# Optimization experiments

Hardware: AMD Instinct MI355X
Metric: run time of the kernel (lower is better)

## Reference

```python
import jax, jax.numpy as jnp
import numpy as np


def _gru_cell(x, h, Wih, Whh, bih, bhh):
    # torch nn.GRU cell math: gates ordered [r, z, n]
    gi = Wih @ x + bih
    gh = Whh @ h + bhh
    ir, iz, inn = jnp.split(gi, 3)
    hr, hz, hn = jnp.split(gh, 3)
    r = jax.nn.sigmoid(ir + hr)
    z = jax.nn.sigmoid(iz + hz)
    n = jnp.tanh(inn + r * hn)
    return (1.0 - z) * n + z * h


def _lrelu(x):
    # torch nn.LeakyReLU default negative_slope=0.01
    return jnp.where(x >= 0, x, 0.01 * x)


def setup_inputs() -> dict:
    key = jax.random.key(0)
    ks = jax.random.split(key, 24)
    V, E, H, C, S, T = 32000, 512, 1024, 2048, 256, 129
    w = lambda k, shape: jax.random.normal(k, shape, jnp.float32) * 0.02
    return {
        "inputs": jax.random.randint(ks[0], (T,), 0, V),
        "h1": jax.random.normal(ks[1], (H,), jnp.float32),
        "h2": jax.random.normal(ks[2], (H,), jnp.float32),
        "projected_keys": jax.random.normal(ks[3], (S, H), jnp.float32),
        "encoder_outputs": jax.random.normal(ks[4], (S, C), jnp.float32),
        "embeds": jax.random.normal(ks[5], (V, E), jnp.float32),
        "Wq": w(ks[6], (H, H)),
        "v_att": w(ks[7], (H,)),
        "W_ih1": w(ks[8], (3 * H, E + C)),
        "W_hh1": w(ks[9], (3 * H, H)),
        "b_ih1": w(ks[10], (3 * H,)),
        "b_hh1": w(ks[11], (3 * H,)),
        "W_ih2": w(ks[12], (3 * H, H + C)),
        "W_hh2": w(ks[13], (3 * H, H)),
        "b_ih2": w(ks[14], (3 * H,)),
        "b_hh2": w(ks[15], (3 * H,)),
        "W_pre": w(ks[16], (H, E + H + C)),
        "b_pre": w(ks[17], (H,)),
        "W_out": w(ks[18], (E, H)),
        "b_out": w(ks[19], (E,)),
    }


def reference(inputs, h1, h2, projected_keys, encoder_outputs, embeds, Wq, v_att,
              W_ih1, W_hh1, b_ih1, b_hh1, W_ih2, W_hh2, b_ih2, b_hh2,
              W_pre, b_pre, W_out, b_out):
    # teacher_forcing = 1.0 -> decoder input at step i is inputs[i] (ground truth)
    emb_seq = embeds[inputs[:-1]]  # [T-1, E]

    def step(carry, emb):
        h1, h2 = carry
        # additive attention: query from top-layer hidden state
        q = Wq @ h2                                     # [H]
        e = jnp.tanh(projected_keys + q) @ v_att        # [S]
        alphas = jax.nn.softmax(e)                      # [S]
        context = alphas @ encoder_outputs              # [C]
        h1n = _gru_cell(jnp.concatenate([emb, context]), h1, W_ih1, W_hh1, b_ih1, b_hh1)
        o1 = _lrelu(h1n)                                # dropout identity (eval)
        h2n = _gru_cell(jnp.concatenate([o1, context]), h2, W_ih2, W_hh2, b_ih2, b_hh2)
        o2 = _lrelu(h2n)
        pre = _lrelu(W_pre @ jnp.concatenate([emb, o2, context]) + b_pre)  # [H]
        out = W_out @ o2 + b_out                        # [E]
        return (h1n, h2n), (out, pre, alphas)

    (h1f, h2f), (outs, pres, alphas) = jax.lax.scan(step, (h1, h2), emb_seq)
    # torch.cat(outputs, dim=1) of [1,1,E] pieces -> [1, T-1, E]
    return outs[None], pres[None], alphas, h1f, h2f
```

## Files before the change

kernel.cpp:

```cpp
#include <hip/hip_runtime.h>

typedef unsigned int uint32;

#define GBLK 256
#define BT 512
#define NSTEP 128

#define CQ   0
#define CGH  1
#define CE   2
#define CCTX 3
#define CH1  4
#define CH2  5
#define QF    1024
#define EF    2048
#define CTXF  2304
#define H1FO  4352
#define H2FO  5376
#define O1F   6400
#define O2F   7424
#define GH1F  8448
#define GH2F  12544

struct Params {
  const int* inputs;
  const float *h1_in, *h2_in, *embeds, *vatt;
  const float *pk, *enc, *Wq, *Wih1, *Whh1, *Wih2, *Whh2, *Wpre, *Wout;
  const float *bih1, *bhh1, *bih2, *bhh2, *bpre, *bout;
  float* out;
  float* ws;
};

__device__ __forceinline__ float blo(uint32 u) { return __uint_as_float(u << 16); }
__device__ __forceinline__ float bhi(uint32 u) { return __uint_as_float(u & 0xffff0000u); }
__device__ __forceinline__ uint32 bfr(float f) {
  uint32 u = __float_as_uint(f);
  return (u + 0x7fffu + ((u >> 16) & 1u)) >> 16;
}

__device__ __forceinline__ float ald(const float* a) {
  return __hip_atomic_load(a, __ATOMIC_RELAXED, __HIP_MEMORY_SCOPE_AGENT);
}
__device__ __forceinline__ void ast(float* a, float v) {
  __hip_atomic_store(a, v, __ATOMIC_RELAXED, __HIP_MEMORY_SCOPE_AGENT);
}

__device__ __forceinline__ float4 cld16(const float* p) {
  float4 r;
  asm volatile("global_load_dwordx4 %0, %1, off sc0 sc1\n\ts_waitcnt vmcnt(0)"
               : "=&v"(r) : "v"(p) : "memory");
  return r;
}

#define VDRAIN() asm volatile("s_waitcnt vmcnt(0)" ::: "memory")

__device__ __forceinline__ void cadd(int* wsi, int c, int b) {
  __hip_atomic_fetch_add(wsi + c * 128 + (b & 7) * 16, 1,
                         __ATOMIC_RELAXED, __HIP_MEMORY_SCOPE_AGENT);
}
__device__ __forceinline__ void cpoll(const int* wsi, int c, int tgt) {
  const int* base = wsi + c * 128;
  for (;;) {
    bool ok = true;
#pragma unroll
    for (int k = 0; k < 8; ++k)
      ok &= (__hip_atomic_load(base + k * 16, __ATOMIC_RELAXED,
                               __HIP_MEMORY_SCOPE_AGENT) >= tgt);
    if (ok) return;
    __builtin_amdgcn_s_sleep(1);
  }
}

__device__ __forceinline__ float wsum(float v) {
#pragma unroll
  for (int o = 32; o; o >>= 1) v += __shfl_xor(v, o, 64);
  return v;
}

__device__ __forceinline__ void ldchunk(const float* W, size_t base, int lane, uint32* r) {
  const float* wf = W + base + lane * 8;
  float4 a = *(const float4*)wf;
  float4 c = *(const float4*)(wf + 4);
  r[0] = bfr(a.x) | (bfr(a.y) << 16);
  r[1] = bfr(a.z) | (bfr(a.w) << 16);
  r[2] = bfr(c.x) | (bfr(c.y) << 16);
  r[3] = bfr(c.z) | (bfr(c.w) << 16);
}

__device__ __forceinline__ float dotchunk(const uint32* r, const float* xc, int lane) {
  const float* x = xc + lane * 8;
  float4 x0 = *(const float4*)x, x1 = *(const float4*)(x + 4);
  return blo(r[0]) * x0.x + bhi(r[0]) * x0.y + blo(r[1]) * x0.z + bhi(r[1]) * x0.w +
         blo(r[2]) * x1.x + bhi(r[2]) * x1.y + blo(r[3]) * x1.z + bhi(r[3]) * x1.w;
}

__device__ __forceinline__ float sigm(float x) { return 1.f / (1.f + expf(-x)); }
__device__ __forceinline__ float lrelu(float x) { return x >= 0.f ? x : 0.01f * x; }

__global__ __launch_bounds__(BT, 2) void dec_cnt_kernel(Params p) {
  __shared__ float sx[8192];
  __shared__ float s_red[8];
  __shared__ float s_part[72];

  const int tid = threadIdx.x;
  const int lane = tid & 63;
  const int w = tid >> 6;
  const int b = blockIdx.x;
  const int gw = b * 8 + w;
  const int i0 = b * 4;
  const int j0 = b * 8;

  int* wsi = (int*)p.ws;

  float* outs = p.out;
  float* pres = p.out + 65536;
  float* alph = p.out + 196608;
  float* h1f = p.out + 229376;
  float* h2f = p.out + 230400;

  uint32 wa[48];
  if (gw < 1024) {
#pragma unroll
    for (int c = 0; c < 7; ++c)
      ldchunk(p.Wpre, (size_t)gw * 3584 + c * 512, lane, wa + 4 * c);
    ldchunk(p.Whh1, (size_t)gw * 1024, lane, wa + 28);
    ldchunk(p.Whh1, (size_t)gw * 1024 + 512, lane, wa + 32);
    ldchunk(p.Whh1, (size_t)(gw + 1024) * 1024, lane, wa + 36);
    ldchunk(p.Whh1, (size_t)(gw + 1024) * 1024 + 512, lane, wa + 40);
    wa[44] = wa[45] = wa[46] = wa[47] = 0u;
  } else {
    const int widx = gw - 1024;
    ldchunk(p.Whh1, (size_t)(2048 + widx) * 1024, lane, wa + 0);
    ldchunk(p.Whh1, (size_t)(2048 + widx) * 1024 + 512, lane, wa + 4);
#pragma unroll
    for (int r = 0; r < 3; ++r) {
      ldchunk(p.Whh2, (size_t)(widx + r * 1024) * 1024, lane, wa + 8 + 8 * r);
      ldchunk(p.Whh2, (size_t)(widx + r * 1024) * 1024 + 512, lane, wa + 12 + 8 * r);
    }
    ldchunk(p.Wq, (size_t)widx * 1024, lane, wa + 32);
    ldchunk(p.Wq, (size_t)widx * 1024 + 512, lane, wa + 36);
    const int wr = widx & 511;
    ldchunk(p.Wout, (size_t)wr * 1024, lane, wa + 40);
    ldchunk(p.Wout, (size_t)wr * 1024 + 512, lane, wa + 44);
  }

  uint32 wd[32];
#pragma unroll
  for (int k = 0; k < 8; ++k) {
    const int mm = w + 8 * k;
    const int mmc = mm < 60 ? mm : 0;
    const int r = mmc / 15, m = mmc % 15, g = m / 5, c = m % 5;
    ldchunk(p.Wih1, (size_t)(g * 1024 + i0 + r) * 2560 + c * 512, lane, wd + 4 * k);
  }

  uint32 we9[36];
#pragma unroll
  for (int k = 0; k < 9; ++k) {
    const int mm = w + 8 * k;
    const int r = mm / 18, m = mm % 18, g = m / 6, c = m % 6;
    ldchunk(p.Wih2, (size_t)(g * 1024 + i0 + r) * 3072 + c * 512, lane, we9 + 4 * k);
  }

  uint32 wenc[4] = {0u, 0u, 0u, 0u};
  float4 pk4 = {0.f, 0.f, 0.f, 0.f}, va4 = {0.f, 0.f, 0.f, 0.f};
  if (tid < 256) {
    const float* er = p.enc + (size_t)tid * 2048 + j0;
    float4 a = *(const float4*)er, c = *(const float4*)(er + 4);
    wenc[0] = bfr(a.x) | (bfr(a.y) << 16);
    wenc[1] = bfr(a.z) | (bfr(a.w) << 16);
    wenc[2] = bfr(c.x) | (bfr(c.y) << 16);
    wenc[3] = bfr(c.z) | (bfr(c.w) << 16);
    pk4 = *(const float4*)(p.pk + (size_t)b * 1024 + 4 * tid);
    va4 = *(const float4*)(p.vatt + 4 * tid);
  }

  if (tid < 4) {
    ast(p.ws + H1FO + i0 + tid, p.h1_in[i0 + tid]);
    ast(p.ws + H2FO + i0 + tid, p.h2_in[i0 + tid]);
  }
  VDRAIN();
  if (tid == 0) { cadd(wsi, CH1, b); cadd(wsi, CH2, b); }

  for (int t = 0; t <= NSTEP; ++t) {
    if (t < NSTEP) {
      if (tid == 0) { cpoll(wsi, CH1, 32 * (t + 1)); cpoll(wsi, CH2, 32 * (t + 1)); }
      __syncthreads();
      if (tid < 256 || b >= 128) {
        const float* hsrc = (tid < 256) ? (p.ws + H1FO + 4 * tid)
                                        : (p.ws + H2FO + 4 * (tid - 256));
        float4 hv = cld16(hsrc);
        *(float4*)&sx[6144 + 4 * tid] = hv;
      }
      __syncthreads();
      if (b >= 128) {
        const int widx = gw - 1024;
        float sq = dotchunk(wa + 32, sx + 7168, lane) + dotchunk(wa + 36, sx + 7680, lane);
        sq = wsum(sq);
        if (lane == 0) ast(p.ws + QF + widx, sq);
        VDRAIN();
        __syncthreads();
        if (tid == 0) cadd(wsi, CQ, b);
        float s = dotchunk(wa + 0, sx + 6144, lane) + dotchunk(wa + 4, sx + 6656, lane);
        s = wsum(s);
        if (lane == 0) ast(p.ws + GH1F + widx * 4 + 2, s + p.bhh1[2048 + widx]);
#pragma unroll
        for (int r = 0; r < 3; ++r) {
          float t2 = dotchunk(wa + 8 + 8 * r, sx + 7168, lane) +
                     dotchunk(wa + 12 + 8 * r, sx + 7680, lane);
          t2 = wsum(t2);
          if (lane == 0) ast(p.ws + GH2F + widx * 4 + r, t2 + p.bhh2[widx + 1024 * r]);
        }
        VDRAIN();
        __syncthreads();
        if (tid == 0) cadd(wsi, CGH, b);
      } else {
        float s1 = dotchunk(wa + 28, sx + 6144, lane) + dotchunk(wa + 32, sx + 6656, lane);
        s1 = wsum(s1);
        if (lane == 0) ast(p.ws + GH1F + gw * 4 + 0, s1 + p.bhh1[gw]);
        float s2 = dotchunk(wa + 36, sx + 6144, lane) + dotchunk(wa + 40, sx + 6656, lane);
        s2 = wsum(s2);
        if (lane == 0) ast(p.ws + GH1F + gw * 4 + 1, s2 + p.bhh1[1024 + gw]);
        VDRAIN();
        __syncthreads();
        if (tid == 0) cadd(wsi, CGH, b);
      }

      if (tid == 0) cpoll(wsi, CQ, 16 * (t + 1));
      __syncthreads();
      if (tid < 256) {
        float4 qv = cld16(p.ws + QF + 4 * tid);
        float acc = va4.x * tanhf(pk4.x + qv.x) + va4.y * tanhf(pk4.y + qv.y) +
                    va4.z * tanhf(pk4.z + qv.z) + va4.w * tanhf(pk4.w + qv.w);
        acc = wsum(acc);
        if (lane == 0) s_red[w] = acc;
      }
      __syncthreads();
      if (tid == 0) {
        float e = s_red[0] + s_red[1] + s_red[2] + s_red[3];
        ast(p.ws + EF + b, e);
        VDRAIN();
        cadd(wsi, CE, b);
      }
    }

    if (t > 0) {
      if (t == NSTEP) {
        if (tid == 0) cpoll(wsi, CH2, 32 * (t + 1));
      }
      __syncthreads();
      if (tid < 256) {
        float4 v = cld16(p.ws + O2F + 4 * tid);
        *(float4*)&sx[2560 + 4 * tid] = v;
      }
      __syncthreads();
      if (gw < 1024) {
        float s = 0.f;
#pragma unroll
        for (int c = 0; c < 7; ++c) {
          const float* xp = (c == 0) ? sx
                          : (c <= 2) ? (sx + 2560 + (c - 1) * 512)
                                     : (sx + 512 + (c - 3) * 512);
          s += dotchunk(wa + 4 * c, xp, lane);
        }
        s = wsum(s);
        if (lane == 0) pres[(size_t)(t - 1) * 1024 + gw] = lrelu(s + p.bpre[gw]);
      } else if (gw - 1024 < 512) {
        const int widx = gw - 1024;
        float so = dotchunk(wa + 40, sx + 2560, lane) + dotchunk(wa + 44, sx + 3072, lane);
        so = wsum(so);
        if (lane == 0) outs[(size_t)(t - 1) * 512 + widx] = so + p.bout[widx];
      }
    }
    if (t == NSTEP) break;

    {
      if (tid == 0) cpoll(wsi, CE, 32 * (t + 1));
      __syncthreads();
      if (tid < 64) {
        float4 ev = cld16(p.ws + EF + 4 * tid);
        *(float4*)&sx[4096 + 4 * tid] = ev;
      }
      __syncthreads();
      float e_i = 0.f, pe = 0.f;
      if (tid < 256) {
        e_i = sx[4096 + tid];
        float mw = e_i;
#pragma unroll
        for (int o = 32; o; o >>= 1) mw = fmaxf(mw, __shfl_xor(mw, o, 64));
        if (lane == 0) s_red[w] = mw;
      }
      __syncthreads();
      float m = fmaxf(fmaxf(s_red[0], s_red[1]), fmaxf(s_red[2], s_red[3]));
      __syncthreads();
      if (tid < 256) {
        pe = expf(e_i - m);
        float zw = wsum(pe);
        if (lane == 0) s_red[w] = zw;
      }
      __syncthreads();
      float Z = s_red[0] + s_red[1] + s_red[2] + s_red[3];
      if (tid < 256) {
        float alpha = pe / Z;
        if (b == 0) alph[(size_t)t * 256 + tid] = alpha;
        float c[8];
        c[0] = alpha * blo(wenc[0]); c[1] = alpha * bhi(wenc[0]);
        c[2] = alpha * blo(wenc[1]); c[3] = alpha * bhi(wenc[1]);
        c[4] = alpha * blo(wenc[2]); c[5] = alpha * bhi(wenc[2]);
        c[6] = alpha * blo(wenc[3]); c[7] = alpha * bhi(wenc[3]);
#pragma unroll
        for (int o = 32; o; o >>= 1) {
#pragma unroll
          for (int j = 0; j < 8; ++j) c[j] += __shfl_xor(c[j], o, 64);
        }
        if (lane == 0) {
#pragma unroll
          for (int j = 0; j < 8; ++j) s_part[w * 8 + j] = c[j];
        }
      }
      __syncthreads();
      if (tid < 8) {
        float cj = s_part[tid] + s_part[8 + tid] + s_part[16 + tid] + s_part[24 + tid];
        ast(p.ws + CTXF + j0 + tid, cj);
      }
      VDRAIN();
      if (tid == 0) cadd(wsi, CCTX, b);
    }

    {
      if (tid == 0) { cpoll(wsi, CCTX, 32 * (t + 1)); cpoll(wsi, CGH, 32 * (t + 1)); }
      __syncthreads();
      const float* embc = p.embeds + (size_t)p.inputs[t] * 512;
      sx[tid] = embc[tid];
      {
        float4 cv = cld16(p.ws + CTXF + 4 * tid);
        *(float4*)&sx[512 + 4 * tid] = cv;
      }
      float4 g1 = {0.f, 0.f, 0.f, 0.f};
      float h1old = 0.f;
      if (tid < 4) {
        g1 = cld16(p.ws + GH1F + (i0 + tid) * 4);
        h1old = ald(p.ws + H1FO + i0 + tid);
      }
      __syncthreads();
#pragma unroll
      for (int k = 0; k < 8; ++k) {
        const int mm = w + 8 * k;
        if (mm < 60) {
          const int c = (mm % 15) % 5;
          float s = dotchunk(wd + 4 * k, sx + c * 512, lane);
          s = wsum(s);
          if (lane == 0) s_part[mm] = s;
        }
      }
      __syncthreads();
      if (tid < 4) {
        const int i = i0 + tid;
        const float* sp = s_part + tid * 15;
        float sr = sp[0] + sp[1] + sp[2] + sp[3] + sp[4];
        float sz = sp[5] + sp[6] + sp[7] + sp[8] + sp[9];
        float sn = sp[10] + sp[11] + sp[12] + sp[13] + sp[14];
        float r = sigm(sr + p.bih1[i] + g1.x);
        float z = sigm(sz + p.bih1[1024 + i] + g1.y);
        float n = tanhf(sn + p.bih1[2048 + i] + r * g1.z);
        float h = (1.f - z) * n + z * h1old;
        ast(p.ws + H1FO + i, h);
        ast(p.ws + O1F + i, lrelu(h));
      }
      VDRAIN();
      if (tid == 0) cadd(wsi, CH1, b);
    }

    {
      if (tid == 0) cpoll(wsi, CH1, 32 * (t + 2));
      __syncthreads();
      if (tid < 256) {
        float4 ov = cld16(p.ws + O1F + 4 * tid);
        *(float4*)&sx[2560 + 4 * tid] = ov;
      }
      float4 g2 = {0.f, 0.f, 0.f, 0.f};
      float h2old = 0.f;
      if (tid < 4) {
        g2 = cld16(p.ws + GH2F + (i0 + tid) * 4);
        h2old = ald(p.ws + H2FO + i0 + tid);
      }
      __syncthreads();
#pragma unroll
      for (int k = 0; k < 9; ++k) {
        const int mm = w + 8 * k;
        const int c = (mm % 18) % 6;
        const float* xp = (c < 2) ? (sx + 2560 + c * 512) : (sx + 512 + (c - 2) * 512);
        float s = dotchunk(we9 + 4 * k, xp, lane);
        s = wsum(s);
        if (lane == 0) s_part[mm] = s;
      }
      __syncthreads();
      if (tid < 4) {
        const int i = i0 + tid;
        const float* sp = s_part + tid * 18;
        float sr = sp[0] + sp[1] + sp[2] + sp[3] + sp[4] + sp[5];
        float sz = sp[6] + sp[7] + sp[8] + sp[9] + sp[10] + sp[11];
        float sn = sp[12] + sp[13] + sp[14] + sp[15] + sp[16] + sp[17];
        float r = sigm(sr + p.bih2[i] + g2.x);
        float z = sigm(sz + p.bih2[1024 + i] + g2.y);
        float n = tanhf(sn + p.bih2[2048 + i] + r * g2.z);
        float h = (1.f - z) * n + z * h2old;
        ast(p.ws + H2FO + i, h);
        ast(p.ws + O2F + i, lrelu(h));
      }
      VDRAIN();
      if (tid == 0) cadd(wsi, CH2, b);
    }
  }

  if (tid < 4) {
    h1f[i0 + tid] = ald(p.ws + H1FO + i0 + tid);
    h2f[i0 + tid] = ald(p.ws + H2FO + i0 + tid);
  }
}

extern "C" void kernel_launch(void* const* d_in, const int* in_sizes, int n_in,
                              void* d_out, int out_size, void* d_ws, size_t ws_size,
                              hipStream_t stream) {
  (void)hipMemsetAsync(d_ws, 0, 4096, stream);

  Params p;
  p.inputs = (const int*)d_in[0];
  p.h1_in = (const float*)d_in[1];
  p.h2_in = (const float*)d_in[2];
  p.pk = (const float*)d_in[3];
  p.enc = (const float*)d_in[4];
  p.embeds = (const float*)d_in[5];
  p.Wq = (const float*)d_in[6];
  p.vatt = (const float*)d_in[7];
  p.Wih1 = (const float*)d_in[8];
  p.Whh1 = (const float*)d_in[9];
  p.bih1 = (const float*)d_in[10];
  p.bhh1 = (const float*)d_in[11];
  p.Wih2 = (const float*)d_in[12];
  p.Whh2 = (const float*)d_in[13];
  p.bih2 = (const float*)d_in[14];
  p.bhh2 = (const float*)d_in[15];
  p.Wpre = (const float*)d_in[16];
  p.bpre = (const float*)d_in[17];
  p.Wout = (const float*)d_in[18];
  p.bout = (const float*)d_in[19];
  p.out = (float*)d_out;
  p.ws = (float*)d_ws;

  void* args[] = {&p};
  hipError_t err = hipLaunchCooperativeKernel((const void*)dec_cnt_kernel,
                                              dim3(GBLK), dim3(BT), args, 0, stream);
  if (err != hipSuccess) {
    dec_cnt_kernel<<<dim3(GBLK), dim3(BT), 0, stream>>>(p);
  }
}
```

Measured before the change: 6.061 ms.

## Replace atomic-counter barriers with per-block epoch flags polled by a wavefront

Swaps the shared fetch-add counters (8 striped slots per phase) for one flag slot per block per phase, written with a plain atomic store of the step epoch. A whole wavefront polls all 256 flags with vector loads and an __all reduction, instead of a single thread looping over atomic loads. The CGH wait is narrowed to just the two producer blocks this block depends on. The aim is to remove atomic RMW contention and cut barrier latency across the 128 steps, at the cost of more polling traffic per wait and a larger workspace reset.

```diff
diff --git a/kernel.cpp b/kernel.cpp
--- a/kernel.cpp
+++ b/kernel.cpp
@@ -12,15 +12,15 @@
 #define CCTX 3
 #define CH1  4
 #define CH2  5
-#define QF    1024
-#define EF    2048
-#define CTXF  2304
-#define H1FO  4352
-#define H2FO  5376
-#define O1F   6400
-#define O2F   7424
-#define GH1F  8448
-#define GH2F  12544
+#define QF    2048
+#define EF    3072
+#define CTXF  3328
+#define H1FO  5376
+#define H2FO  6400
+#define O1F   7424
+#define O2F   8448
+#define GH1F  9472
+#define GH2F  13568
 
 struct Params {
   const int* inputs;
@@ -44,6 +44,12 @@
 __device__ __forceinline__ void ast(float* a, float v) {
   __hip_atomic_store(a, v, __ATOMIC_RELAXED, __HIP_MEMORY_SCOPE_AGENT);
 }
+__device__ __forceinline__ int aldi(const int* a) {
+  return __hip_atomic_load(a, __ATOMIC_RELAXED, __HIP_MEMORY_SCOPE_AGENT);
+}
+__device__ __forceinline__ void asti(int* a, int v) {
+  __hip_atomic_store(a, v, __ATOMIC_RELAXED, __HIP_MEMORY_SCOPE_AGENT);
+}
 
 __device__ __forceinline__ float4 cld16(const float* p) {
   float4 r;
@@ -51,22 +57,56 @@
                : "=&v"(r) : "v"(p) : "memory");
   return r;
 }
+__device__ __forceinline__ int4 cldi4(const int* p) {
+  int4 r;
+  asm volatile("global_load_dwordx4 %0, %1, off sc0 sc1\n\ts_waitcnt vmcnt(0)"
+               : "=&v"(r) : "v"(p) : "memory");
+  return r;
+}
 
 #define VDRAIN() asm volatile("s_waitcnt vmcnt(0)" ::: "memory")
 
-__device__ __forceinline__ void cadd(int* wsi, int c, int b) {
-  __hip_atomic_fetch_add(wsi + c * 128 + (b & 7) * 16, 1,
-                         __ATOMIC_RELAXED, __HIP_MEMORY_SCOPE_AGENT);
-}
-__device__ __forceinline__ void cpoll(const int* wsi, int c, int tgt) {
-  const int* base = wsi + c * 128;
+__device__ __forceinline__ void fst(int* flg, int c, int slot, int v) {
+  asti(flg + c * 256 + slot, v);
+}
+__device__ __forceinline__ void fpoll256(const int* flg, int c, int tgt, int lane) {
+  const int* base = flg + c * 256 + lane * 4;
   for (;;) {
-    bool ok = true;
-#pragma unroll
-    for (int k = 0; k < 8; ++k)
-      ok &= (__hip_atomic_load(base + k * 16, __ATOMIC_RELAXED,
-                               __HIP_MEMORY_SCOPE_AGENT) >= tgt);
-    if (ok) return;
+    int4 v = cldi4(base);
+    bool ok = v.x >= tgt && v.y >= tgt && v.z >= tgt && v.w >= tgt;
+    if (__all(ok)) return;
+    __builtin_amdgcn_s_sleep(1);
+  }
+}
+__device__ __forceinline__ void fpoll2x256(const int* flg, int c1, int c2, int tgt, int lane) {
+  const int* b1 = flg + c1 * 256 + lane * 4;
+  const int* b2 = flg + c2 * 256 + lane * 4;
+  for (;;) {
+    int4 v, u;
+    asm volatile("global_load_dwordx4 %0, %2, off sc0 sc1\n\t"
+                 "global_load_dwordx4 %1, %3, off sc0 sc1\n\t"
+                 "s_waitcnt vmcnt(0)"
+                 : "=&v"(v), "=&v"(u) : "v"(b1), "v"(b2) : "memory");
+    bool ok = v.x >= tgt && v.y >= tgt && v.z >= tgt && v.w >= tgt &&
+              u.x >= tgt && u.y >= tgt && u.z >= tgt && u.w >= tgt;
+    if (__all(ok)) return;
+    __builtin_amdgcn_s_sleep(1);
+  }
+}
+__device__ __forceinline__ void fpoll128hi(const int* flg, int c, int tgt, int lane) {
+  const int* base = flg + c * 256 + 128 + (lane & 31) * 4;
+  for (;;) {
+    int4 v = cldi4(base);
+    bool ok = v.x >= tgt && v.y >= tgt && v.z >= tgt && v.w >= tgt;
+    if (__all(ok)) return;
+    __builtin_amdgcn_s_sleep(1);
+  }
+}
+__device__ __forceinline__ void fpollp2(const int* flg, int c, int s0, int s1, int tgt) {
+  const int* a0 = flg + c * 256 + s0;
+  const int* a1 = flg + c * 256 + s1;
+  for (;;) {
+    if (aldi(a0) >= tgt && aldi(a1) >= tgt) return;
     __builtin_amdgcn_s_sleep(1);
   }
 }
@@ -97,7 +137,7 @@
 __device__ __forceinline__ float sigm(float x) { return 1.f / (1.f + expf(-x)); }
 __device__ __forceinline__ float lrelu(float x) { return x >= 0.f ? x : 0.01f * x; }
 
-__global__ __launch_bounds__(BT, 2) void dec_cnt_kernel(Params p) {
+__global__ __launch_bounds__(BT, 2) void dec_flag_kernel(Params p) {
   __shared__ float sx[8192];
   __shared__ float s_red[8];
   __shared__ float s_part[72];
@@ -110,7 +150,7 @@
   const int i0 = b * 4;
   const int j0 = b * 8;
 
-  int* wsi = (int*)p.ws;
+  int* flg = (int*)p.ws;
 
   float* outs = p.out;
   float* pres = p.out + 65536;
@@ -179,11 +219,11 @@
     ast(p.ws + H2FO + i0 + tid, p.h2_in[i0 + tid]);
   }
   VDRAIN();
-  if (tid == 0) { cadd(wsi, CH1, b); cadd(wsi, CH2, b); }
+  if (tid == 0) { fst(flg, CH1, b, 1); fst(flg, CH2, b, 1); }
 
   for (int t = 0; t <= NSTEP; ++t) {
     if (t < NSTEP) {
-      if (tid == 0) { cpoll(wsi, CH1, 32 * (t + 1)); cpoll(wsi, CH2, 32 * (t + 1)); }
+      if (w == 0) fpoll2x256(flg, CH1, CH2, t + 1, lane);
       __syncthreads();
       if (tid < 256 || b >= 128) {
         const float* hsrc = (tid < 256) ? (p.ws + H1FO + 4 * tid)
@@ -199,7 +239,7 @@
         if (lane == 0) ast(p.ws + QF + widx, sq);
         VDRAIN();
         __syncthreads();
-        if (tid == 0) cadd(wsi, CQ, b);
+        if (tid == 0) fst(flg, CQ, b, t + 1);
         float s = dotchunk(wa + 0, sx + 6144, lane) + dotchunk(wa + 4, sx + 6656, lane);
         s = wsum(s);
         if (lane == 0) ast(p.ws + GH1F + widx * 4 + 2, s + p.bhh1[2048 + widx]);
@@ -212,7 +252,7 @@
         }
         VDRAIN();
         __syncthreads();
-        if (tid == 0) cadd(wsi, CGH, b);
+        if (tid == 0) fst(flg, CGH, b, t + 1);
       } else {
         float s1 = dotchunk(wa + 28, sx + 6144, lane) + dotchunk(wa + 32, sx + 6656, lane);
         s1 = wsum(s1);
@@ -222,10 +262,10 @@
         if (lane == 0) ast(p.ws + GH1F + gw * 4 + 1, s2 + p.bhh1[1024 + gw]);
         VDRAIN();
         __syncthreads();
-        if (tid == 0) cadd(wsi, CGH, b);
-      }
-
-      if (tid == 0) cpoll(wsi, CQ, 16 * (t + 1));
+        if (tid == 0) fst(flg, CGH, b, t + 1);
+      }
+
+      if (w == 0) fpoll128hi(flg, CQ, t + 1, lane);
       __syncthreads();
       if (tid < 256) {
         float4 qv = cld16(p.ws + QF + 4 * tid);
@@ -239,13 +279,13 @@
         float e = s_red[0] + s_red[1] + s_red[2] + s_red[3];
         ast(p.ws + EF + b, e);
         VDRAIN();
-        cadd(wsi, CE, b);
+        fst(flg, CE, b, t + 1);
       }
     }
 
     if (t > 0) {
       if (t == NSTEP) {
-        if (tid == 0) cpoll(wsi, CH2, 32 * (t + 1));
+        if (w == 0) fpoll256(flg, CH2, t + 1, lane);
       }
       __syncthreads();
       if (tid < 256) {
@@ -274,7 +314,7 @@
     if (t == NSTEP) break;
 
     {
-      if (tid == 0) cpoll(wsi, CE, 32 * (t + 1));
+      if (w == 0) fpoll256(flg, CE, t + 1, lane);
       __syncthreads();
       if (tid < 64) {
         float4 ev = cld16(p.ws + EF + 4 * tid);
@@ -323,11 +363,14 @@
         ast(p.ws + CTXF + j0 + tid, cj);
       }
       VDRAIN();
-      if (tid == 0) cadd(wsi, CCTX, b);
+      if (tid == 0) fst(flg, CCTX, b, t + 1);
     }
 
     {
-      if (tid == 0) { cpoll(wsi, CCTX, 32 * (t + 1)); cpoll(wsi, CGH, 32 * (t + 1)); }
+      if (w == 0) {
+        fpoll256(flg, CCTX, t + 1, lane);
+        fpollp2(flg, CGH, b >> 1, 128 + (b >> 1), t + 1);
+      }
       __syncthreads();
       const float* embc = p.embeds + (size_t)p.inputs[t] * 512;
       sx[tid] = embc[tid];
@@ -367,11 +410,11 @@
         ast(p.ws + O1F + i, lrelu(h));
       }
       VDRAIN();
-      if (tid == 0) cadd(wsi, CH1, b);
+      if (tid == 0) fst(flg, CH1, b, t + 2);
     }
 
     {
-      if (tid == 0) cpoll(wsi, CH1, 32 * (t + 2));
+      if (w == 0) fpoll256(flg, CH1, t + 2, lane);
       __syncthreads();
       if (tid < 256) {
         float4 ov = cld16(p.ws + O1F + 4 * tid);
@@ -408,7 +451,7 @@
         ast(p.ws + O2F + i, lrelu(h));
       }
       VDRAIN();
-      if (tid == 0) cadd(wsi, CH2, b);
+      if (tid == 0) fst(flg, CH2, b, t + 2);
     }
   }
 
@@ -421,7 +464,7 @@
 extern "C" void kernel_launch(void* const* d_in, const int* in_sizes, int n_in,
                               void* d_out, int out_size, void* d_ws, size_t ws_size,
                               hipStream_t stream) {
-  (void)hipMemsetAsync(d_ws, 0, 4096, stream);
+  (void)hipMemsetAsync(d_ws, 0, 8192, stream);
 
   Params p;
   p.inputs = (const int*)d_in[0];
@@ -448,9 +491,9 @@
   p.ws = (float*)d_ws;
 
   void* args[] = {&p};
-  hipError_t err = hipLaunchCooperativeKernel((const void*)dec_cnt_kernel,
+  hipError_t err = hipLaunchCooperativeKernel((const void*)dec_flag_kernel,
                                               dim3(GBLK), dim3(BT), args, 0, stream);
   if (err != hipSuccess) {
-    dec_cnt_kernel<<<dim3(GBLK), dim3(BT), 0, stream>>>(p);
-  }
-}
+    dec_flag_kernel<<<dim3(GBLK), dim3(BT), 0, stream>>>(p);
+  }
+}
```

Result: slower. 7.231 ms (+19.3%).
